# Kernel optimization log

Measured on AMD Instinct MI355X. Metric: run time of the kernel, lower is better.

## Reference

```python
import jax, jax.numpy as jnp
import numpy as np

N = 300000   # total nodes
C = 32       # hidden states
M = 64       # discrete label alphabet
NGEN = 8     # number of generative models
G = 8192     # number of graphs


def setup_inputs() -> dict:
    key = jax.random.key(0)
    k1, k2, k3, k4 = jax.random.split(key, 4)
    B = jax.random.uniform(k1, (C, M, NGEN), minval=-5.0, maxval=5.0, dtype=jnp.float32)
    Pi = jax.random.uniform(k2, (C, NGEN), minval=-5.0, maxval=5.0, dtype=jnp.float32)
    x = jax.random.randint(k3, (N,), 0, M)
    batch = jnp.sort(jax.random.randint(k4, (N,), 0, G))
    return {"B": B, "Pi": Pi, "x": x, "batch": batch, "num_graphs": G}


def reference(B, Pi, x, batch, num_graphs):
    # softmax reparameterization: over M for B, over C for Pi (per generator)
    sm_B = jax.nn.softmax(B, axis=1)          # (C, M, n_gen)
    sm_Pi = jax.nn.softmax(Pi, axis=0)        # (C, n_gen)
    # gather per-node emission probs, then joint with prior -> (N, C, n_gen)
    numerator = sm_Pi[None, :, :] * jnp.transpose(sm_B[:, x, :], (1, 0, 2))
    posterior = numerator / numerator.sum(axis=1, keepdims=True)  # (N, C, n_gen)
    likelihood = (posterior * jnp.log(numerator)).sum(axis=1)     # (N, n_gen)
    # scatter-sum per graph
    likelihood = jax.ops.segment_sum(likelihood, batch, num_segments=num_graphs)  # (G, n_gen)
    h_vals = posterior.max(axis=1, keepdims=True)   # (N, 1, n_gen)
    h_idx = posterior.argmax(axis=1)                # (N, n_gen)
    return likelihood, h_vals, h_idx
```

## Files before the change

### kernel.cpp

```cpp
#include <hip/hip_runtime.h>

#define C_DIM 32
#define M_DIM 64
#define NG    8
#define TAB   (M_DIM * NG)
#define ST    9
#define SPB   1024


__global__ void __launch_bounds__(256)
cgmm_partials(const float* __restrict__ B, const float* __restrict__ Pi,
              const int* __restrict__ batch,
              float* __restrict__ Sexp, float* __restrict__ lsePi,
              int* __restrict__ starts, int N, int G) {
    const int tid = threadIdx.x;
    const int bid = blockIdx.x;

    if (bid < C_DIM) {
        __shared__ float row_s[M_DIM * NG];
        const float* row = B + bid * (M_DIM * NG);
        row_s[tid]       = row[tid];
        row_s[tid + 256] = row[tid + 256];
        __syncthreads();
        if (tid < NG) {
            float s = 0.f;
            #pragma unroll
            for (int m = 0; m < M_DIM; ++m) s += __expf(row_s[m * NG + tid]);
            Sexp[bid * NG + tid] = s;
        }
        return;
    }
    if (bid == C_DIM) {
        __shared__ float pi_s[C_DIM * NG];
        pi_s[tid] = Pi[tid];
        __syncthreads();
        if (tid < NG) {
            float s = 0.f;
            #pragma unroll
            for (int c = 0; c < C_DIM; ++c) s += __expf(pi_s[c * NG + tid]);
            lsePi[tid] = __logf(s);
        }
        return;
    }

    const int base = (bid - C_DIM - 1) * SPB;
    for (int i = tid; i < SPB; i += 256) {
        const int n = base + i;
        if (n >= N) break;
        const int bn = batch[n];
        if (n == 0) {
            for (int j = 0; j <= bn; ++j) starts[j] = 0;
        } else {
            const int bp = batch[n - 1];
            for (int j = bp + 1; j <= bn; ++j) starts[j] = n;
        }
        if (n == N - 1) {
            for (int j = bn + 1; j <= G; ++j) starts[j] = N;
        }
    }
}

__global__ void __launch_bounds__(512)
cgmm_tables(const float* __restrict__ B, const float* __restrict__ Pi,
            const float* __restrict__ Sexp, const float* __restrict__ lsePi,
            float* __restrict__ tab) {
    __shared__ float K_s[C_DIM * NG];
    const int tid = threadIdx.x;
    if (tid < C_DIM * NG)
        K_s[tid] = Pi[tid] - __logf(Sexp[tid]) - lsePi[tid & 7];
    __syncthreads();

    const int g = tid & 7;
    float L[C_DIM];
    float best = -1e30f; int bidx = 0;
    #pragma unroll
    for (int c = 0; c < C_DIM; ++c) {
        float v = B[c * (M_DIM * NG) + tid] + K_s[c * NG + g];
        L[c] = v;
        if (v > best) { best = v; bidx = c; }
    }
    float se = 0.f, la = 0.f;
    #pragma unroll
    for (int c = 0; c < C_DIM; ++c) {
        float e = __expf(L[c] - best);
        se += e; la += e * L[c];
    }
    tab[tid]           = la / se;
    tab[TAB + tid]     = 1.f / se;
    tab[2 * TAB + tid] = (float)bidx;
}

__global__ void __launch_bounds__(256)
cgmm_write(const int* __restrict__ x, const int* __restrict__ starts,
           const float* __restrict__ tab,
           float* __restrict__ out_like, float* __restrict__ out_hv,
           float* __restrict__ out_hi, int G) {
    __shared__ float like_s[M_DIM * ST];
    __shared__ float hval_s[M_DIM * ST];
    __shared__ float hidx_s[M_DIM * ST];
    const int tid = threadIdx.x;
    for (int i = tid; i < TAB; i += 256) {
        const int p = (i >> 3) * ST + (i & 7);
        like_s[p] = tab[i];
        hval_s[p] = tab[TAB + i];
        hidx_s[p] = tab[2 * TAB + i];
    }
    __syncthreads();

    const int j = blockIdx.x * 4 + (tid >> 6);
    if (j >= G) return;
    const int start = starts[j];
    const int end   = starts[j + 1];

    const int slot = (tid >> 3) & 7;
    const int g    = tid & 7;

    float acc = 0.f;
    for (int n = start + slot; n < end; n += 8) {
        const int xm = x[n];
        const int p  = xm * ST + g;
        acc += like_s[p];
        out_hv[(size_t)n * NG + g] = hval_s[p];
        out_hi[(size_t)n * NG + g] = hidx_s[p];
    }
    acc += __shfl_xor(acc, 8);
    acc += __shfl_xor(acc, 16);
    acc += __shfl_xor(acc, 32);
    if ((tid & 63) < NG) out_like[(size_t)j * NG + g] = acc;
}

extern "C" void kernel_launch(void* const* d_in, const int* in_sizes, int n_in,
                              void* d_out, int out_size, void* d_ws, size_t ws_size,
                              hipStream_t stream) {
    const float* B     = (const float*)d_in[0];
    const float* Pi    = (const float*)d_in[1];
    const int*   x     = (const int*)d_in[2];
    const int*   batch = (const int*)d_in[3];
    const int N = in_sizes[2];
    const int G = (out_size - 2 * N * NG) / NG;

    float* tab    = (float*)d_ws;
    float* Sexp   = (float*)((char*)d_ws + 8192);
    float* lsePi  = (float*)((char*)d_ws + 9216);
    int*   starts = (int*)((char*)d_ws + 16384);

    float* out_like = (float*)d_out;
    float* out_hv   = out_like + (size_t)G * NG;
    float* out_hi   = out_hv + (size_t)N * NG;

    const int nsb = (N + SPB - 1) / SPB;

    cgmm_partials<<<C_DIM + 1 + nsb, 256, 0, stream>>>(B, Pi, batch, Sexp,
                                                       lsePi, starts, N, G);
    cgmm_tables<<<1, 512, 0, stream>>>(B, Pi, Sexp, lsePi, tab);
    cgmm_write<<<(G + 3) / 4, 256, 0, stream>>>(x, starts, tab, out_like,
                                                out_hv, out_hi, G);
}
```

Baseline: 20.03 us.

## Vectorize per-node output writes with float4 and shuffle-broadcast labels

The write kernel now loads each 64-node chunk of labels with one coalesced load per wavefront and broadcasts them through shuffles. Each lane writes half a node's 8 outputs as a float4, so stores are wider and fewer. The likelihood sum is computed separately from the shuffled labels. Blocks grow to 512 threads covering 8 graphs each, which halves the number of blocks doing the table staging, at the cost of more shuffles and several scalar shared-memory reads per float4.

```diff
diff --git a/kernel.cpp b/kernel.cpp
--- a/kernel.cpp
+++ b/kernel.cpp
@@ -90,7 +90,7 @@
     tab[2 * TAB + tid] = (float)bidx;
 }
 
-__global__ void __launch_bounds__(256)
+__global__ void __launch_bounds__(512)
 cgmm_write(const int* __restrict__ x, const int* __restrict__ starts,
            const float* __restrict__ tab,
            float* __restrict__ out_like, float* __restrict__ out_hv,
@@ -99,7 +99,7 @@
     __shared__ float hval_s[M_DIM * ST];
     __shared__ float hidx_s[M_DIM * ST];
     const int tid = threadIdx.x;
-    for (int i = tid; i < TAB; i += 256) {
+    for (int i = tid; i < TAB; i += 512) {
         const int p = (i >> 3) * ST + (i & 7);
         like_s[p] = tab[i];
         hval_s[p] = tab[TAB + i];
@@ -107,26 +107,51 @@
     }
     __syncthreads();
 
-    const int j = blockIdx.x * 4 + (tid >> 6);
+    const int j = blockIdx.x * 8 + (tid >> 6);
     if (j >= G) return;
     const int start = starts[j];
     const int end   = starts[j + 1];
 
-    const int slot = (tid >> 3) & 7;
-    const int g    = tid & 7;
+    const int lane = tid & 63;
+    const int slot = lane >> 3;
+    const int g    = lane & 7;
+
+    float4* hv4 = (float4*)out_hv;
+    float4* hi4 = (float4*)out_hi;
 
     float acc = 0.f;
-    for (int n = start + slot; n < end; n += 8) {
-        const int xm = x[n];
-        const int p  = xm * ST + g;
-        acc += like_s[p];
-        out_hv[(size_t)n * NG + g] = hval_s[p];
-        out_hi[(size_t)n * NG + g] = hidx_s[p];
+    for (int cb = start; cb < end; cb += 64) {
+        const int cnt = end - cb;
+        const int xv  = (cb + lane < end) ? x[cb + lane] : 0;
+
+        #pragma unroll
+        for (int s = 0; s < 2; ++s) {
+            const int f    = s * 64 + lane;
+            const int node = f >> 1;
+            const int h    = (f & 1) * 4;
+            const int xm   = __shfl(xv, node);
+            if (node < cnt) {
+                const int p = xm * ST + h;
+                float4 v, w;
+                v.x = hval_s[p];     v.y = hval_s[p + 1];
+                v.z = hval_s[p + 2]; v.w = hval_s[p + 3];
+                w.x = hidx_s[p];     w.y = hidx_s[p + 1];
+                w.z = hidx_s[p + 2]; w.w = hidx_s[p + 3];
+                hv4[(size_t)cb * 2 + f] = v;
+                hi4[(size_t)cb * 2 + f] = w;
+            }
+        }
+        #pragma unroll
+        for (int t = 0; t < 8; ++t) {
+            const int node = slot + 8 * t;
+            const int xm   = __shfl(xv, node);
+            if (node < cnt) acc += like_s[xm * ST + g];
+        }
     }
     acc += __shfl_xor(acc, 8);
     acc += __shfl_xor(acc, 16);
     acc += __shfl_xor(acc, 32);
-    if ((tid & 63) < NG) out_like[(size_t)j * NG + g] = acc;
+    if (lane < NG) out_like[(size_t)j * NG + g] = acc;
 }
 
 extern "C" void kernel_launch(void* const* d_in, const int* in_sizes, int n_in,
@@ -153,6 +178,6 @@
     cgmm_partials<<<C_DIM + 1 + nsb, 256, 0, stream>>>(B, Pi, batch, Sexp,
                                                        lsePi, starts, N, G);
     cgmm_tables<<<1, 512, 0, stream>>>(B, Pi, Sexp, lsePi, tab);
-    cgmm_write<<<(G + 3) / 4, 256, 0, stream>>>(x, starts, tab, out_like,
+    cgmm_write<<<(G + 7) / 8, 512, 0, stream>>>(x, starts, tab, out_like,
                                                 out_hv, out_hi, G);
 }
```

Result: no change. 19.74 us (-1.4%).
